# Kernel tuning notes

Hardware: AMD Instinct MI355X
Metric: run time of the kernel (lower is better)

## Reference

```python
import jax, jax.numpy as jnp
import numpy as np

B = 4096          # batch
IN = 4096         # in_features
OUT = 4096        # out_features
MASK_DENSITY = 0.1

def setup_inputs() -> dict:
    key = jax.random.key(0)
    k1, k2, k3, k4, k5 = jax.random.split(key, 5)
    x = jax.random.normal(k1, (B, IN), dtype=jnp.float32)
    # truncated-normal-ish init, std 0.1 (plain normal scaled is fine for a numeric baseline)
    weight = jax.random.normal(k2, (OUT, IN), dtype=jnp.float32) * 0.1
    bound = 1.0 / np.sqrt(IN)
    bias = jax.random.uniform(k3, (OUT,), dtype=jnp.float32, minval=-bound, maxval=bound)
    mask = jax.random.bernoulli(k4, MASK_DENSITY, (OUT, IN))  # bool, fixed sparsity pattern
    residual_connection = jax.random.randint(k5, (OUT,), 0, IN, dtype=jnp.int32)
    return {"x": x, "weight": weight, "bias": bias, "mask": mask,
            "residual_connection": residual_connection}

def reference(x, weight, bias, mask, residual_connection):
    # out = relu(x @ (mask * W)^T + b) + x[:, residual_connection]
    w_masked = jnp.where(mask, weight, 0.0)              # [OUT, IN]
    out = x @ w_masked.T + bias                          # [B, OUT]
    out = jax.nn.relu(out)
    out = jnp.take(x, residual_connection, axis=1) + out # gathered residual add
    return out
```

## Files before the change

kernel.cpp:

```cpp
#include <hip/hip_runtime.h>
#include <hip/hip_bf16.h>
#include <stdint.h>

#define B_ROWS 4096
#define IN_F   4096
#define OUT_F  4096

#define BM 256
#define BN 256
#define BK 64
#define NKT (IN_F / BK)

typedef float  f32x4  __attribute__((ext_vector_type(4)));
typedef short  bf16x8 __attribute__((ext_vector_type(8)));
typedef unsigned short u16x4 __attribute__((ext_vector_type(4)));

#define AS1 __attribute__((address_space(1)))
#define AS3 __attribute__((address_space(3)))

template<int N> struct IC { static constexpr int v = N; };

__device__ __forceinline__ uint16_t f2bf_rne(float f) {
    uint32_t u = __float_as_uint(f);
    uint32_t r = u + 0x7fffu + ((u >> 16) & 1u);
    return (uint16_t)(r >> 16);
}
__device__ __forceinline__ float bf2f(uint16_t h) {
    return __uint_as_float(((uint32_t)h) << 16);
}

__global__ __launch_bounds__(256) void prep_kernel(
    const float* __restrict__ x, uint16_t* __restrict__ xb, uint16_t* __restrict__ xbT,
    const float* __restrict__ w, const void* __restrict__ mraw, uint16_t* __restrict__ wb)
{
    const int tid = threadIdx.x;
    const int blk = blockIdx.x;

    if (blk < 4096) {
        __shared__ float t[64][65];
        const int r0 = (blk >> 6) * 64;
        const int c0 = (blk & 63) * 64;
        const int lr = tid >> 4;
        const int lc4 = (tid & 15) * 4;

#pragma unroll
        for (int p = 0; p < 4; ++p) {
            const int row = p * 16 + lr;
            float4 v = *(const float4*)(x + (size_t)(r0 + row) * IN_F + c0 + lc4);
            ushort4 o;
            o.x = f2bf_rne(v.x); o.y = f2bf_rne(v.y);
            o.z = f2bf_rne(v.z); o.w = f2bf_rne(v.w);
            *(ushort4*)(xb + (size_t)(r0 + row) * IN_F + c0 + lc4) = o;
            t[row][lc4 + 0] = v.x; t[row][lc4 + 1] = v.y;
            t[row][lc4 + 2] = v.z; t[row][lc4 + 3] = v.w;
        }
        __syncthreads();
#pragma unroll
        for (int p = 0; p < 4; ++p) {
            const int c = p * 16 + lr;
            ushort4 o;
            o.x = f2bf_rne(t[lc4 + 0][c]);
            o.y = f2bf_rne(t[lc4 + 1][c]);
            o.z = f2bf_rne(t[lc4 + 2][c]);
            o.w = f2bf_rne(t[lc4 + 3][c]);
            *(ushort4*)(xbT + (size_t)(c0 + c) * B_ROWS + r0 + lc4) = o;
        }
    } else {
        __shared__ int wflag[4];
        uint32_t mword = ((const uint32_t*)mraw)[tid];
        unsigned long long bal = __ballot((mword & 0xFFFFFF00u) != 0);
        if ((tid & 63) == 0) wflag[tid >> 6] = (bal != 0ull);
        __syncthreads();
        const int flag = wflag[0] | wflag[1] | wflag[2] | wflag[3];

        const size_t e = ((size_t)(blk - 4096)) * 2048 + (size_t)tid * 8;
        float4 v0 = *(const float4*)(w + e);
        float4 v1 = *(const float4*)(w + e + 4);
        int m[8];
        if (flag) {
            uint2 mm = *(const uint2*)((const uint8_t*)mraw + e);
#pragma unroll
            for (int j = 0; j < 4; ++j) m[j]     = (mm.x >> (8 * j)) & 0xff;
#pragma unroll
            for (int j = 0; j < 4; ++j) m[4 + j] = (mm.y >> (8 * j)) & 0xff;
        } else {
            const int* mp = (const int*)mraw + e;
            int4 a = *(const int4*)mp;
            int4 b = *(const int4*)(mp + 4);
            m[0] = a.x; m[1] = a.y; m[2] = a.z; m[3] = a.w;
            m[4] = b.x; m[5] = b.y; m[6] = b.z; m[7] = b.w;
        }
        bf16x8 o;
        o[0] = m[0] ? (short)f2bf_rne(v0.x) : (short)0;
        o[1] = m[1] ? (short)f2bf_rne(v0.y) : (short)0;
        o[2] = m[2] ? (short)f2bf_rne(v0.z) : (short)0;
        o[3] = m[3] ? (short)f2bf_rne(v0.w) : (short)0;
        o[4] = m[4] ? (short)f2bf_rne(v1.x) : (short)0;
        o[5] = m[5] ? (short)f2bf_rne(v1.y) : (short)0;
        o[6] = m[6] ? (short)f2bf_rne(v1.z) : (short)0;
        o[7] = m[7] ? (short)f2bf_rne(v1.w) : (short)0;
        *(bf16x8*)(wb + e) = o;
    }
}

__device__ __forceinline__ bf16x8 ds_read128(uint32_t off) {
    bf16x8 r;
    asm volatile("ds_read_b128 %0, %1" : "=v"(r) : "v"(off));
    return r;
}
#define LDSOFF(p) ((uint32_t)(uintptr_t)(AS3 void*)(p))

__global__ __launch_bounds__(512, 2) void gemm_kernel(
    const uint16_t* __restrict__ xb, const uint16_t* __restrict__ wb,
    const uint16_t* __restrict__ xbT, const float* __restrict__ bias,
    const int* __restrict__ rc, float* __restrict__ out)
{
    __shared__ alignas(16) uint16_t Abuf[2][2][128 * BK];
    __shared__ alignas(16) uint16_t Bbuf[2][2][128 * BK];
    __shared__ float bias_s[BN];
    __shared__ int   rc_s[BN];

    const int tid = threadIdx.x;

    const int bid = blockIdx.x;
    const int wg  = (bid & 7) * 32 + (bid >> 3);
    const int row0 = (wg >> 4) * BM;
    const int col0 = (wg & 15) * BN;

    const int wave = tid >> 6, lane = tid & 63;
    const int wm = wave >> 2;
    const int wn = wave & 3;
    const int bh = wn >> 1;
    const int quad = lane >> 4, l16 = lane & 15;
    const int swr = (l16 & 7) << 3;
    const int e0  = (quad << 3) ^ swr;
    const uint32_t kd = (uint32_t)(((e0 ^ 32) - e0) * 2);

    const uint32_t aOff0 = LDSOFF(&Abuf[0][wm][0]) + (uint32_t)((l16 * BK + e0) * 2);
    const uint32_t aOff1 = LDSOFF(&Abuf[1][wm][0]) + (uint32_t)((l16 * BK + e0) * 2);
    const uint32_t bOff0 = LDSOFF(&Bbuf[0][bh][0]) + (uint32_t)((((wn & 1) * 64 + l16) * BK + e0) * 2);
    const uint32_t bOff1 = LDSOFF(&Bbuf[1][bh][0]) + (uint32_t)((((wn & 1) * 64 + l16) * BK + e0) * 2);

    const int srow = tid >> 3;
    const int ssw  = ((tid & 7) ^ (srow & 7)) << 3;
    const uint16_t* pA0 = xb + (size_t)(row0 + srow) * IN_F + ssw;
    const uint16_t* pB0 = wb + (size_t)(col0 + srow) * IN_F + ssw;
    const uint16_t* pA1 = pA0 + (size_t)128 * IN_F;
    const uint16_t* pB1 = pB0 + (size_t)128 * IN_F;

    auto stage = [&](const uint16_t* src, uint16_t* ldsdst, size_t ko) {
        __builtin_amdgcn_global_load_lds((const AS1 void*)(src + ko),
                                         (AS3 void*)(ldsdst + tid * 8), 16, 0, 0);
        __builtin_amdgcn_global_load_lds((const AS1 void*)(src + ko + (size_t)64 * IN_F),
                                         (AS3 void*)(ldsdst + tid * 8 + 4096), 16, 0, 0);
    };

    if (tid < BN) {
        __builtin_amdgcn_global_load_lds((const AS1 void*)(bias + col0 + tid),
                                         (AS3 void*)(bias_s + tid), 4, 0, 0);
        __builtin_amdgcn_global_load_lds((const AS1 void*)(rc + col0 + tid),
                                         (AS3 void*)(rc_s + tid), 4, 0, 0);
    }

    f32x4 acc[8][4];
#pragma unroll
    for (int mi = 0; mi < 8; ++mi)
#pragma unroll
        for (int ni = 0; ni < 4; ++ni)
            acc[mi][ni] = (f32x4){0.f, 0.f, 0.f, 0.f};

    stage(pA0, &Abuf[0][0][0], 0);
    stage(pA1, &Abuf[0][1][0], 0);
    stage(pB0, &Bbuf[0][0][0], 0);
    stage(pB1, &Bbuf[0][1][0], 0);

#define LGKM(n) do { asm volatile("s_waitcnt lgkmcnt(" #n ")" ::: "memory"); \
                     __builtin_amdgcn_sched_barrier(0); } while (0)

    auto tile = [&](auto curc, int t) {
        constexpr int CUR = decltype(curc)::v;
        constexpr int NXT = CUR ^ 1;
        const uint32_t aB = CUR ? aOff1 : aOff0;
        const uint32_t bB = CUR ? bOff1 : bOff0;
        const size_t koff = (size_t)(t + 1) * BK;

        bf16x8 b[4], b2[4], a0[4], a1[4], a2[4], a3[4];

        asm volatile("s_waitcnt vmcnt(0)" ::: "memory");
        __builtin_amdgcn_s_barrier();
        __builtin_amdgcn_sched_barrier(0);

#pragma unroll
        for (int ni = 0; ni < 4; ++ni) b[ni]  = ds_read128(bB + ni * 2048);
#pragma unroll
        for (int m = 0; m < 4; ++m)    a0[m]  = ds_read128(aB + m * 2048);
#pragma unroll
        for (int m = 0; m < 4; ++m)    a1[m]  = ds_read128(aB + (4 + m) * 2048);
        stage(pA0, &Abuf[NXT][0][0], koff);
        stage(pA1, &Abuf[NXT][1][0], koff);

        LGKM(4);
        __builtin_amdgcn_s_setprio(1);
#pragma unroll
        for (int m = 0; m < 4; ++m)
#pragma unroll
            for (int ni = 0; ni < 4; ++ni)
                acc[m][ni] = __builtin_amdgcn_mfma_f32_16x16x32_bf16(a0[m], b[ni], acc[m][ni], 0, 0, 0);
        __builtin_amdgcn_s_setprio(0);

#pragma unroll
        for (int m = 0; m < 4; ++m)    a2[m]  = ds_read128(aB + m * 2048 + kd);
        stage(pB0, &Bbuf[NXT][0][0], koff);
        stage(pB1, &Bbuf[NXT][1][0], koff);

        LGKM(4);
        __builtin_amdgcn_s_setprio(1);
#pragma unroll
        for (int m = 0; m < 4; ++m)
#pragma unroll
            for (int ni = 0; ni < 4; ++ni)
                acc[4 + m][ni] = __builtin_amdgcn_mfma_f32_16x16x32_bf16(a1[m], b[ni], acc[4 + m][ni], 0, 0, 0);
        __builtin_amdgcn_s_setprio(0);

#pragma unroll
        for (int ni = 0; ni < 4; ++ni) b2[ni] = ds_read128(bB + ni * 2048 + kd);
#pragma unroll
        for (int m = 0; m < 4; ++m)    a3[m]  = ds_read128(aB + (4 + m) * 2048 + kd);

        LGKM(4);
        __builtin_amdgcn_s_setprio(1);
#pragma unroll
        for (int m = 0; m < 4; ++m)
#pragma unroll
            for (int ni = 0; ni < 4; ++ni)
                acc[m][ni] = __builtin_amdgcn_mfma_f32_16x16x32_bf16(a2[m], b2[ni], acc[m][ni], 0, 0, 0);
        __builtin_amdgcn_s_setprio(0);

        LGKM(0);
        __builtin_amdgcn_s_setprio(1);
#pragma unroll
        for (int m = 0; m < 4; ++m)
#pragma unroll
            for (int ni = 0; ni < 4; ++ni)
                acc[4 + m][ni] = __builtin_amdgcn_mfma_f32_16x16x32_bf16(a3[m], b2[ni], acc[4 + m][ni], 0, 0, 0);
        __builtin_amdgcn_s_setprio(0);
    };

    for (int tt = 0; tt < NKT; tt += 2) {
        tile(IC<0>{}, tt);
        tile(IC<1>{}, tt + 1);
    }
#undef LGKM

#pragma unroll
    for (int ni = 0; ni < 4; ++ni) {
        const int lcol = wn * 64 + ni * 16 + l16;
        const int gcol = col0 + lcol;
        const float bv = bias_s[lcol];
        const int   rv = rc_s[lcol];
#pragma unroll
        for (int mi = 0; mi < 8; ++mi) {
            const int grow0 = row0 + wm * 128 + mi * 16 + quad * 4;
            u16x4 xq = *(const u16x4*)(xbT + (size_t)rv * B_ROWS + grow0);
#pragma unroll
            for (int r = 0; r < 4; ++r) {
                float v = fmaxf(acc[mi][ni][r] + bv, 0.0f) + bf2f(xq[r]);
                out[(size_t)(grow0 + r) * OUT_F + gcol] = v;
            }
        }
    }
}

extern "C" void kernel_launch(void* const* d_in, const int* in_sizes, int n_in,
                              void* d_out, int out_size, void* d_ws, size_t ws_size,
                              hipStream_t stream) {
    const float* x    = (const float*)d_in[0];
    const float* w    = (const float*)d_in[1];
    const float* bias = (const float*)d_in[2];
    const void*  mask = (const void*)d_in[3];
    const int*   rc   = (const int*)d_in[4];
    float* out = (float*)d_out;

    uint16_t* xb   = (uint16_t*)d_ws;
    uint16_t* wb   = xb  + (size_t)B_ROWS * IN_F;
    uint16_t* xbT  = wb  + (size_t)OUT_F * IN_F;

    prep_kernel<<<4096 + 8192, 256, 0, stream>>>(x, xb, xbT, w, mask, wb);

    gemm_kernel<<<dim3((B_ROWS / BM) * (OUT_F / BN)), dim3(512), 0, stream>>>(
        xb, wb, xbT, bias, rc, out);
}
```

Before: 337.2 us.

## Prefetch next-tile A fragment across barrier and coarsen weight-prep blocks

The GEMM main loop now loads the first A fragment for the next k-tile during the current tile's last MFMA group. A mid-tile vmcnt wait plus barrier makes sure the next buffer's A data has landed before that read. LDS reads use immediate offsets on precomputed base addresses, which cuts per-read address arithmetic. The weight-masking prep path now has each block process four chunks, shrinking its grid from 8192 to 2048 blocks. The price is an extra barrier per tile and more live registers.

```diff
diff --git a/kernel.cpp b/kernel.cpp
--- a/kernel.cpp
+++ b/kernel.cpp
@@ -73,41 +73,42 @@
         __syncthreads();
         const int flag = wflag[0] | wflag[1] | wflag[2] | wflag[3];
 
-        const size_t e = ((size_t)(blk - 4096)) * 2048 + (size_t)tid * 8;
-        float4 v0 = *(const float4*)(w + e);
-        float4 v1 = *(const float4*)(w + e + 4);
-        int m[8];
-        if (flag) {
-            uint2 mm = *(const uint2*)((const uint8_t*)mraw + e);
-#pragma unroll
-            for (int j = 0; j < 4; ++j) m[j]     = (mm.x >> (8 * j)) & 0xff;
-#pragma unroll
-            for (int j = 0; j < 4; ++j) m[4 + j] = (mm.y >> (8 * j)) & 0xff;
-        } else {
-            const int* mp = (const int*)mraw + e;
-            int4 a = *(const int4*)mp;
-            int4 b = *(const int4*)(mp + 4);
-            m[0] = a.x; m[1] = a.y; m[2] = a.z; m[3] = a.w;
-            m[4] = b.x; m[5] = b.y; m[6] = b.z; m[7] = b.w;
+#pragma unroll
+        for (int it = 0; it < 4; ++it) {
+            const size_t c = (size_t)(blk - 4096) + (size_t)it * 2048;
+            const size_t e = c * 2048 + (size_t)tid * 8;
+            float4 v0 = *(const float4*)(w + e);
+            float4 v1 = *(const float4*)(w + e + 4);
+            int m[8];
+            if (flag) {
+                uint2 mm = *(const uint2*)((const uint8_t*)mraw + e);
+#pragma unroll
+                for (int j = 0; j < 4; ++j) m[j]     = (mm.x >> (8 * j)) & 0xff;
+#pragma unroll
+                for (int j = 0; j < 4; ++j) m[4 + j] = (mm.y >> (8 * j)) & 0xff;
+            } else {
+                const int* mp = (const int*)mraw + e;
+                int4 a = *(const int4*)mp;
+                int4 b = *(const int4*)(mp + 4);
+                m[0] = a.x; m[1] = a.y; m[2] = a.z; m[3] = a.w;
+                m[4] = b.x; m[5] = b.y; m[6] = b.z; m[7] = b.w;
+            }
+            bf16x8 o;
+            o[0] = m[0] ? (short)f2bf_rne(v0.x) : (short)0;
+            o[1] = m[1] ? (short)f2bf_rne(v0.y) : (short)0;
+            o[2] = m[2] ? (short)f2bf_rne(v0.z) : (short)0;
+            o[3] = m[3] ? (short)f2bf_rne(v0.w) : (short)0;
+            o[4] = m[4] ? (short)f2bf_rne(v1.x) : (short)0;
+            o[5] = m[5] ? (short)f2bf_rne(v1.y) : (short)0;
+            o[6] = m[6] ? (short)f2bf_rne(v1.z) : (short)0;
+            o[7] = m[7] ? (short)f2bf_rne(v1.w) : (short)0;
+            *(bf16x8*)(wb + e) = o;
         }
-        bf16x8 o;
-        o[0] = m[0] ? (short)f2bf_rne(v0.x) : (short)0;
-        o[1] = m[1] ? (short)f2bf_rne(v0.y) : (short)0;
-        o[2] = m[2] ? (short)f2bf_rne(v0.z) : (short)0;
-        o[3] = m[3] ? (short)f2bf_rne(v0.w) : (short)0;
-        o[4] = m[4] ? (short)f2bf_rne(v1.x) : (short)0;
-        o[5] = m[5] ? (short)f2bf_rne(v1.y) : (short)0;
-        o[6] = m[6] ? (short)f2bf_rne(v1.z) : (short)0;
-        o[7] = m[7] ? (short)f2bf_rne(v1.w) : (short)0;
-        *(bf16x8*)(wb + e) = o;
     }
 }
 
-__device__ __forceinline__ bf16x8 ds_read128(uint32_t off) {
-    bf16x8 r;
-    asm volatile("ds_read_b128 %0, %1" : "=v"(r) : "v"(off));
-    return r;
-}
+#define DSR(dst, base, OFS) \
+    asm volatile("ds_read_b128 %0, %1 offset:" #OFS : "=v"(dst) : "v"(base))
 #define LDSOFF(p) ((uint32_t)(uintptr_t)(AS3 void*)(p))
 
 __global__ __launch_bounds__(512, 2) void gemm_kernel(
@@ -136,10 +137,11 @@
     const int e0  = (quad << 3) ^ swr;
     const uint32_t kd = (uint32_t)(((e0 ^ 32) - e0) * 2);
 
-    const uint32_t aOff0 = LDSOFF(&Abuf[0][wm][0]) + (uint32_t)((l16 * BK + e0) * 2);
-    const uint32_t aOff1 = LDSOFF(&Abuf[1][wm][0]) + (uint32_t)((l16 * BK + e0) * 2);
-    const uint32_t bOff0 = LDSOFF(&Bbuf[0][bh][0]) + (uint32_t)((((wn & 1) * 64 + l16) * BK + e0) * 2);
-    const uint32_t bOff1 = LDSOFF(&Bbuf[1][bh][0]) + (uint32_t)((((wn & 1) * 64 + l16) * BK + e0) * 2);
+    const uint32_t aB0  = LDSOFF(&Abuf[0][wm][0]) + (uint32_t)((l16 * BK + e0) * 2);
+    const uint32_t aB1  = LDSOFF(&Abuf[1][wm][0]) + (uint32_t)((l16 * BK + e0) * 2);
+    const uint32_t bB0  = LDSOFF(&Bbuf[0][bh][0]) + (uint32_t)((((wn & 1) * 64 + l16) * BK + e0) * 2);
+    const uint32_t bB1  = LDSOFF(&Bbuf[1][bh][0]) + (uint32_t)((((wn & 1) * 64 + l16) * BK + e0) * 2);
+    const uint32_t aB0k = aB0 + kd, aB1k = aB1 + kd, bB0k = bB0 + kd, bB1k = bB1 + kd;
 
     const int srow = tid >> 3;
     const int ssw  = ((tid & 7) ^ (srow & 7)) << 3;
@@ -173,6 +175,15 @@
     stage(pA1, &Abuf[0][1][0], 0);
     stage(pB0, &Bbuf[0][0][0], 0);
     stage(pB1, &Bbuf[0][1][0], 0);
+    asm volatile("s_waitcnt vmcnt(0)" ::: "memory");
+    __builtin_amdgcn_s_barrier();
+    __builtin_amdgcn_sched_barrier(0);
+
+    bf16x8 a0p[4];
+    DSR(a0p[0], aB0, 0);
+    DSR(a0p[1], aB0, 2048);
+    DSR(a0p[2], aB0, 4096);
+    DSR(a0p[3], aB0, 6144);
 
 #define LGKM(n) do { asm volatile("s_waitcnt lgkmcnt(" #n ")" ::: "memory"); \
                      __builtin_amdgcn_sched_barrier(0); } while (0)
@@ -180,22 +191,21 @@
     auto tile = [&](auto curc, int t) {
         constexpr int CUR = decltype(curc)::v;
         constexpr int NXT = CUR ^ 1;
-        const uint32_t aB = CUR ? aOff1 : aOff0;
-        const uint32_t bB = CUR ? bOff1 : bOff0;
+        const uint32_t aB  = CUR ? aB1  : aB0;
+        const uint32_t aBk = CUR ? aB1k : aB0k;
+        const uint32_t bB  = CUR ? bB1  : bB0;
+        const uint32_t bBk = CUR ? bB1k : bB0k;
+        const uint32_t aN  = CUR ? aB0  : aB1;
         const size_t koff = (size_t)(t + 1) * BK;
 
-        bf16x8 b[4], b2[4], a0[4], a1[4], a2[4], a3[4];
+        bf16x8 b[4], b2[4], a1[4], a2[4], a3[4];
 
         asm volatile("s_waitcnt vmcnt(0)" ::: "memory");
         __builtin_amdgcn_s_barrier();
         __builtin_amdgcn_sched_barrier(0);
 
-#pragma unroll
-        for (int ni = 0; ni < 4; ++ni) b[ni]  = ds_read128(bB + ni * 2048);
-#pragma unroll
-        for (int m = 0; m < 4; ++m)    a0[m]  = ds_read128(aB + m * 2048);
-#pragma unroll
-        for (int m = 0; m < 4; ++m)    a1[m]  = ds_read128(aB + (4 + m) * 2048);
+        DSR(b[0], bB, 0); DSR(b[1], bB, 2048); DSR(b[2], bB, 4096); DSR(b[3], bB, 6144);
+        DSR(a1[0], aB, 8192); DSR(a1[1], aB, 10240); DSR(a1[2], aB, 12288); DSR(a1[3], aB, 14336);
         stage(pA0, &Abuf[NXT][0][0], koff);
         stage(pA1, &Abuf[NXT][1][0], koff);
 
@@ -205,11 +215,10 @@
         for (int m = 0; m < 4; ++m)
 #pragma unroll
             for (int ni = 0; ni < 4; ++ni)
-                acc[m][ni] = __builtin_amdgcn_mfma_f32_16x16x32_bf16(a0[m], b[ni], acc[m][ni], 0, 0, 0);
+                acc[m][ni] = __builtin_amdgcn_mfma_f32_16x16x32_bf16(a0p[m], b[ni], acc[m][ni], 0, 0, 0);
         __builtin_amdgcn_s_setprio(0);
 
-#pragma unroll
-        for (int m = 0; m < 4; ++m)    a2[m]  = ds_read128(aB + m * 2048 + kd);
+        DSR(a2[0], aBk, 0); DSR(a2[1], aBk, 2048); DSR(a2[2], aBk, 4096); DSR(a2[3], aBk, 6144);
         stage(pB0, &Bbuf[NXT][0][0], koff);
         stage(pB1, &Bbuf[NXT][1][0], koff);
 
@@ -222,10 +231,12 @@
                 acc[4 + m][ni] = __builtin_amdgcn_mfma_f32_16x16x32_bf16(a1[m], b[ni], acc[4 + m][ni], 0, 0, 0);
         __builtin_amdgcn_s_setprio(0);
 
-#pragma unroll
-        for (int ni = 0; ni < 4; ++ni) b2[ni] = ds_read128(bB + ni * 2048 + kd);
-#pragma unroll
-        for (int m = 0; m < 4; ++m)    a3[m]  = ds_read128(aB + (4 + m) * 2048 + kd);
+        DSR(b2[0], bBk, 0); DSR(b2[1], bBk, 2048); DSR(b2[2], bBk, 4096); DSR(b2[3], bBk, 6144);
+        DSR(a3[0], aBk, 8192); DSR(a3[1], aBk, 10240); DSR(a3[2], aBk, 12288); DSR(a3[3], aBk, 14336);
+
+        asm volatile("s_waitcnt vmcnt(4)" ::: "memory");
+        __builtin_amdgcn_s_barrier();
+        __builtin_amdgcn_sched_barrier(0);
 
         LGKM(4);
         __builtin_amdgcn_s_setprio(1);
@@ -236,7 +247,9 @@
                 acc[m][ni] = __builtin_amdgcn_mfma_f32_16x16x32_bf16(a2[m], b2[ni], acc[m][ni], 0, 0, 0);
         __builtin_amdgcn_s_setprio(0);
 
-        LGKM(0);
+        DSR(a0p[0], aN, 0); DSR(a0p[1], aN, 2048); DSR(a0p[2], aN, 4096); DSR(a0p[3], aN, 6144);
+
+        LGKM(4);
         __builtin_amdgcn_s_setprio(1);
 #pragma unroll
         for (int m = 0; m < 4; ++m)
@@ -285,7 +298,7 @@
     uint16_t* wb   = xb  + (size_t)B_ROWS * IN_F;
     uint16_t* xbT  = wb  + (size_t)OUT_F * IN_F;
 
-    prep_kernel<<<4096 + 8192, 256, 0, stream>>>(x, xb, xbT, w, mask, wb);
+    prep_kernel<<<4096 + 2048, 256, 0, stream>>>(x, xb, xbT, w, mask, wb);
 
     gemm_kernel<<<dim3((B_ROWS / BM) * (OUT_F / BN)), dim3(512), 0, stream>>>(
         xb, wb, xbT, bias, rc, out);
```

Measured after the change: 348.7 us. 3.4% more time.
